# Optimization experiments

Hardware: AMD Instinct MI355X
Metric: run time of the kernel (lower is better)

Reference implementation:

```python
import jax, jax.numpy as jnp
import numpy as np

# Static module configuration (matches init_kwargs)
B, C_IN, H, W = 128, 64, 32, 32
C_OUT = 128
K = 3
PAD = 1
STRIDE = 1
OUT_H = (H + 2 * PAD - K) // STRIDE + 1  # 32
OUT_W = (W + 2 * PAD - K) // STRIDE + 1  # 32
L = OUT_H * OUT_W                        # 1024
IN_FEAT = C_IN * K * K                   # 576


def setup_inputs() -> dict:
    key = jax.random.key(0)
    k1, k2, k3 = jax.random.split(key, 3)
    x = jax.random.normal(k1, (B, C_IN, H, W), dtype=jnp.float32)
    # kaiming-uniform-ish scale: 1/sqrt(fan_in)
    bound = 1.0 / np.sqrt(IN_FEAT)
    weight = jax.random.uniform(k2, (L, IN_FEAT, C_OUT), dtype=jnp.float32,
                                minval=-bound, maxval=bound)
    bias = jax.random.uniform(k3, (L, C_OUT), dtype=jnp.float32,
                              minval=-bound, maxval=bound)
    return {"x": x, "weight": weight, "bias": bias}


def _unfold(x):
    """torch.nn.Unfold equivalent: returns (B, L, C*K*K), channel-major feature order."""
    xp = jnp.pad(x, ((0, 0), (0, 0), (PAD, PAD), (PAD, PAD)))
    cols = []
    for i in range(K):
        for j in range(K):
            cols.append(xp[:, :, i:i + OUT_H * STRIDE:STRIDE,
                               j:j + OUT_W * STRIDE:STRIDE])
    # (B, C, K*K, out_h, out_w) -> feature index = c*K*K + i*K + j (torch unfold order)
    p = jnp.stack(cols, axis=2)
    p = p.reshape(x.shape[0], C_IN * K * K, L)
    return p.transpose(0, 2, 1)  # (B, L, in_feat)


def reference(x, weight, bias):
    patches = _unfold(x)                                  # (B, L, in_feat)
    out = jnp.einsum('bli,lio->blo', patches, weight)     # per-location matmul
    out = out + bias[None]                                # (B, L, out_ch)
    out = out.transpose(0, 2, 1).reshape(x.shape[0], C_OUT, OUT_H, OUT_W)
    out = jax.nn.relu(out)
    # MaxPool2d(2, 2)
    Bn = out.shape[0]
    out = out.reshape(Bn, C_OUT, OUT_H // 2, 2, OUT_W // 2, 2).max(axis=(3, 5))
    return out
```

## Files before the change

### kernel.cpp

```cpp
#include <hip/hip_runtime.h>

#define BB   128
#define CI   64
#define HH   32
#define WW   32
#define CO   128
#define IF   576
#define OW   32
#define XH   34
#define XW   34
#define XP_CB    (CI*BB)
#define XP_ELEMS ((size_t)XH*XW*CI*BB)
#define BKC  64
#define NCH  36
#define LDK  72
#define COB  64

#define BAR() asm volatile("s_waitcnt lgkmcnt(0)\n\ts_barrier" ::: "memory")

using short8 = __attribute__((ext_vector_type(8))) short;
using f32x4  = __attribute__((ext_vector_type(4))) float;

__device__ __forceinline__ unsigned short f2bf(float f) {
  union { float f; unsigned int u; } v; v.f = f;
  unsigned int u = v.u;
  u = (u + 0x7FFFu + ((u >> 16) & 1u)) >> 16;
  return (unsigned short)u;
}

__device__ __forceinline__ unsigned int cvt_pk_bf16(float lo, float hi) {
  unsigned int r;
  asm("v_cvt_pk_bf16_f32 %0, %1, %2" : "=v"(r) : "v"(lo), "v"(hi));
  return r;
}

__global__ __launch_bounds__(256) void transpose_x(
    const float* __restrict__ x, unsigned short* __restrict__ xp) {
  const int c = blockIdx.x >> 5;
  const int h = blockIdx.x & 31;
  __shared__ __align__(16) unsigned short tile[32][136];
  const int t = threadIdx.x;
  const int w = t & 31, b0 = t >> 5;
#pragma unroll
  for (int p = 0; p < 16; ++p) {
    int b = b0 + p * 8;
    float v = x[(((size_t)b * CI + c) * HH + h) * WW + w];
    tile[w][b] = f2bf(v);
  }
  __syncthreads();
  const int w2 = t >> 3;
  const int bb = (t & 7) * 16;
  const unsigned short* src = &tile[w2][bb];
  unsigned short* dst = xp + ((size_t)(h + 1) * XW + (w2 + 1)) * XP_CB + c * BB + bb;
  *(uint4*)(dst)     = *(const uint4*)(src);
  *(uint4*)(dst + 8) = *(const uint4*)(src + 8);

  if (blockIdx.x < 132) {
    int s = blockIdx.x, hh, wh;
    if (s < 34)      { hh = 0;  wh = s; }
    else if (s < 68) { hh = 33; wh = s - 34; }
    else             { int k = s - 68; hh = 1 + (k >> 1); wh = (k & 1) * 33; }
    uint4 z; z.x = z.y = z.z = z.w = 0u;
    uint4* p = (uint4*)(xp + ((size_t)hh * XW + wh) * XP_CB) + t;
#pragma unroll
    for (int q = 0; q < 4; ++q) p[q * 256] = z;
  }
}

__global__ __launch_bounds__(512, 4) void local_gemm_pool(
    const float* __restrict__ Wt, const float* __restrict__ bias,
    const unsigned short* __restrict__ xp, float* __restrict__ out) {
  __shared__ __align__(16) unsigned short Asl[2][BB][LDK];
  __shared__ __align__(16) unsigned short Bsl[2][COB][LDK];

  const int tid  = threadIdx.x;
  const int lane = tid & 63;
  const int wave = tid >> 6;

  const int bidx = blockIdx.x;
  const int x8 = bidx & 7, j = bidx >> 3;
  const int coh = j & 1;
  const int pw  = (j >> 1) & 15;
  const int ph  = 2 * x8 + (j >> 5);
  const int co0 = coh * COB;

  const int sa = tid & 127;
  const int ka = tid >> 7;
  const int sb = tid & 63;
  const int kb = tid >> 6;

  const int r16 = lane & 15;
  const int q8  = (lane >> 4) * 8;
  const int m0  = (wave >> 2) * 64;
  const int n0  = (wave & 3) * 16;

  f32x4 acc[4] = {};
  f32x4 rmx[4] = {};

  float          breg0[8], breg1[8];
  unsigned short areg0[16], areg1[16];

  auto issue = [&](int it, float* br, unsigned short* ar) {
    const int loc = it / 9, kc = it % 9;
    const int di = kc / 3, dj = kc % 3;
    const int oh = 2 * ph + (loc >> 1), ow = 2 * pw + (loc & 1);
    const int l  = oh * OW + ow;
    const float* wp = Wt + ((size_t)l * IF + (size_t)(kb * 8) * 9 + kc) * CO
                         + co0 + sb;
#pragma unroll
    for (int i = 0; i < 8; ++i) br[i] = wp[(size_t)i * 9 * CO];
    const unsigned short* ap = xp + ((size_t)(oh + di) * XW + (ow + dj)) * XP_CB
                                  + (ka * 16) * BB + sa;
#pragma unroll
    for (int i = 0; i < 16; ++i) ar[i] = ap[i * BB];
  };

  auto writeLds = [&](int it, const float* br, const unsigned short* ar) {
    const int bufI = it & 1;
    uint4 vb;
    vb.x = cvt_pk_bf16(br[0], br[1]);
    vb.y = cvt_pk_bf16(br[2], br[3]);
    vb.z = cvt_pk_bf16(br[4], br[5]);
    vb.w = cvt_pk_bf16(br[6], br[7]);
    *(uint4*)&Bsl[bufI][sb][kb * 8] = vb;
#pragma unroll
    for (int p = 0; p < 2; ++p) {
      short8 va;
#pragma unroll
      for (int i = 0; i < 8; ++i) va[i] = (short)ar[p * 8 + i];
      *(short8*)&Asl[bufI][sa][ka * 16 + p * 8] = va;
    }
  };

  auto computeChunk = [&](int it) {
    const int bufI = it & 1;
#pragma unroll
    for (int h = 0; h < 2; ++h) {
      const int col = h * 32 + q8;
      short8 af[4], bf;
#pragma unroll
      for (int tm = 0; tm < 4; ++tm)
        af[tm] = *(const short8*)&Asl[bufI][m0 + tm * 16 + r16][col];
      bf = *(const short8*)&Bsl[bufI][n0 + r16][col];
#pragma unroll
      for (int tm = 0; tm < 4; ++tm)
        acc[tm] = __builtin_amdgcn_mfma_f32_16x16x32_bf16(af[tm], bf, acc[tm], 0, 0, 0);
    }
  };

  auto finishLoc = [&](int loc) {
    const int oh = 2 * ph + (loc >> 1), ow = 2 * pw + (loc & 1);
    const int l  = oh * OW + ow;
    const float bv = bias[l * CO + co0 + n0 + r16];
#pragma unroll
    for (int tm = 0; tm < 4; ++tm)
#pragma unroll
      for (int e = 0; e < 4; ++e) {
        float v = acc[tm][e] + bv;
        v = v > 0.f ? v : 0.f;
        rmx[tm][e] = fmaxf(rmx[tm][e], v);
        acc[tm][e] = 0.f;
      }
  };

  issue(0, breg0, areg0);
  issue(1, breg1, areg1);
  writeLds(0, breg0, areg0);
  issue(2, breg0, areg0);
  BAR();

  for (int it2 = 0; it2 < NCH; it2 += 2) {
    computeChunk(it2);
    writeLds(it2 + 1, breg1, areg1);
    if (it2 + 3 < NCH) issue(it2 + 3, breg1, areg1);
    if (it2 % 9 == 8) finishLoc(it2 / 9);
    BAR();
    const int ito = it2 + 1;
    computeChunk(ito);
    if (ito + 1 < NCH) writeLds(ito + 1, breg0, areg0);
    if (ito + 3 < NCH) issue(ito + 3, breg0, areg0);
    if (ito % 9 == 8) finishLoc(ito / 9);
    BAR();
  }

  float* op = out + (ph * 16 + pw);
  const int col = co0 + n0 + r16;
#pragma unroll
  for (int tm = 0; tm < 4; ++tm)
#pragma unroll
    for (int e = 0; e < 4; ++e) {
      const int row = m0 + tm * 16 + (lane >> 4) * 4 + e;
      op[((size_t)row * CO + col) * 256] = rmx[tm][e];
    }
}

extern "C" void kernel_launch(void* const* d_in, const int* in_sizes, int n_in,
                              void* d_out, int out_size, void* d_ws, size_t ws_size,
                              hipStream_t stream) {
  (void)in_sizes; (void)n_in; (void)out_size; (void)ws_size;
  const float* x  = (const float*)d_in[0];
  const float* w  = (const float*)d_in[1];
  const float* bs = (const float*)d_in[2];
  float* out = (float*)d_out;
  unsigned short* xp = (unsigned short*)d_ws;

  transpose_x<<<dim3(CI * HH), dim3(256), 0, stream>>>(x, xp);
  local_gemm_pool<<<dim3(512), dim3(512), 0, stream>>>(w, bs, xp, out);
}
```

Baseline: 454.0 us.

## Reorder pooled-window slots to share input tiles across the four output locations

The loop now walks the 36 (location, tap) slots in an order grouped by input pixel, so each of the 16 distinct input positions in the 4x4 receptive field is loaded into LDS once and reused by every location that needs it. Previously 36 A tiles were loaded. Four accumulator sets are kept live, one per pooled location, and bias, ReLU and max-pool are applied once at the end. The loop is fully unrolled with constexpr schedule tables. The cost is higher accumulator register pressure, which may hurt occupancy at launch bounds 512,4.

```diff
diff --git a/kernel.cpp b/kernel.cpp
--- a/kernel.cpp
+++ b/kernel.cpp
@@ -11,15 +11,24 @@
 #define XW   34
 #define XP_CB    (CI*BB)
 #define XP_ELEMS ((size_t)XH*XW*CI*BB)
-#define BKC  64
-#define NCH  36
 #define LDK  72
 #define COB  64
+#define NSLOT 36
+#define NGRP  16
 
 #define BAR() asm volatile("s_waitcnt lgkmcnt(0)\n\ts_barrier" ::: "memory")
 
 using short8 = __attribute__((ext_vector_type(8))) short;
 using f32x4  = __attribute__((ext_vector_type(4))) float;
+
+__device__ constexpr int SLOC[NSLOT] = {0,0,1,0,1,1,0,2,0,1,2,3,0,1,2,3,1,3,
+                                        0,2,0,1,2,3,0,1,2,3,1,3,2,2,3,2,3,3};
+__device__ constexpr int STAP[NSLOT] = {0,1,0,2,1,2,3,0,4,3,1,0,5,4,2,1,5,2,
+                                        6,3,7,6,4,3,8,7,5,4,8,5,6,7,6,8,7,8};
+__device__ constexpr int GRP[NSLOT]  = {0,1,1,2,2,3,4,4,5,5,5,5,6,6,6,6,7,7,
+                                        8,8,9,9,9,9,10,10,10,10,11,11,12,13,13,14,14,15};
+__device__ constexpr bool ISLAST[NSLOT] = {1,0,1,0,1,1,0,1,0,0,0,1,0,0,0,1,0,1,
+                                           0,1,0,0,0,1,0,0,0,1,0,1,1,0,1,0,1,1};
 
 __device__ __forceinline__ unsigned short f2bf(float f) {
   union { float f; unsigned int u; } v; v.f = f;
@@ -94,28 +103,22 @@
   const int m0  = (wave >> 2) * 64;
   const int n0  = (wave & 3) * 16;
 
-  f32x4 acc[4] = {};
-  f32x4 rmx[4] = {};
+  f32x4 acc[4][4] = {};
 
   float          breg0[8], breg1[8];
-  unsigned short areg0[16], areg1[16];
-
-  auto issue = [&](int it, float* br, unsigned short* ar) {
-    const int loc = it / 9, kc = it % 9;
-    const int di = kc / 3, dj = kc % 3;
+  unsigned short areg[16];
+
+  auto issueB = [&](int it, float* br) {
+    const int loc = SLOC[it], kc = STAP[it];
     const int oh = 2 * ph + (loc >> 1), ow = 2 * pw + (loc & 1);
     const int l  = oh * OW + ow;
     const float* wp = Wt + ((size_t)l * IF + (size_t)(kb * 8) * 9 + kc) * CO
                          + co0 + sb;
 #pragma unroll
     for (int i = 0; i < 8; ++i) br[i] = wp[(size_t)i * 9 * CO];
-    const unsigned short* ap = xp + ((size_t)(oh + di) * XW + (ow + dj)) * XP_CB
-                                  + (ka * 16) * BB + sa;
-#pragma unroll
-    for (int i = 0; i < 16; ++i) ar[i] = ap[i * BB];
-  };
-
-  auto writeLds = [&](int it, const float* br, const unsigned short* ar) {
+  };
+
+  auto writeLdsB = [&](int it, const float* br) {
     const int bufI = it & 1;
     uint4 vb;
     vb.x = cvt_pk_bf16(br[0], br[1]);
@@ -123,74 +126,81 @@
     vb.z = cvt_pk_bf16(br[4], br[5]);
     vb.w = cvt_pk_bf16(br[6], br[7]);
     *(uint4*)&Bsl[bufI][sb][kb * 8] = vb;
+  };
+
+  auto issueA = [&](int g) {
+    const int u = g >> 2, v = g & 3;
+    const unsigned short* ap = xp + ((size_t)(2 * ph + u) * XW + (2 * pw + v)) * XP_CB
+                                  + (ka * 16) * BB + sa;
+#pragma unroll
+    for (int i = 0; i < 16; ++i) areg[i] = ap[i * BB];
+  };
+
+  auto writeLdsA = [&](int g) {
+    const int bufI = g & 1;
 #pragma unroll
     for (int p = 0; p < 2; ++p) {
       short8 va;
 #pragma unroll
-      for (int i = 0; i < 8; ++i) va[i] = (short)ar[p * 8 + i];
+      for (int i = 0; i < 8; ++i) va[i] = (short)areg[p * 8 + i];
       *(short8*)&Asl[bufI][sa][ka * 16 + p * 8] = va;
     }
   };
 
-  auto computeChunk = [&](int it) {
-    const int bufI = it & 1;
+  auto computeSlot = [&](int it) {
+    const int Ab = GRP[it] & 1, Bb = it & 1, loc = SLOC[it];
 #pragma unroll
     for (int h = 0; h < 2; ++h) {
       const int col = h * 32 + q8;
       short8 af[4], bf;
 #pragma unroll
       for (int tm = 0; tm < 4; ++tm)
-        af[tm] = *(const short8*)&Asl[bufI][m0 + tm * 16 + r16][col];
-      bf = *(const short8*)&Bsl[bufI][n0 + r16][col];
+        af[tm] = *(const short8*)&Asl[Ab][m0 + tm * 16 + r16][col];
+      bf = *(const short8*)&Bsl[Bb][n0 + r16][col];
 #pragma unroll
       for (int tm = 0; tm < 4; ++tm)
-        acc[tm] = __builtin_amdgcn_mfma_f32_16x16x32_bf16(af[tm], bf, acc[tm], 0, 0, 0);
-    }
-  };
-
-  auto finishLoc = [&](int loc) {
-    const int oh = 2 * ph + (loc >> 1), ow = 2 * pw + (loc & 1);
-    const int l  = oh * OW + ow;
-    const float bv = bias[l * CO + co0 + n0 + r16];
-#pragma unroll
-    for (int tm = 0; tm < 4; ++tm)
-#pragma unroll
-      for (int e = 0; e < 4; ++e) {
-        float v = acc[tm][e] + bv;
-        v = v > 0.f ? v : 0.f;
-        rmx[tm][e] = fmaxf(rmx[tm][e], v);
-        acc[tm][e] = 0.f;
-      }
-  };
-
-  issue(0, breg0, areg0);
-  issue(1, breg1, areg1);
-  writeLds(0, breg0, areg0);
-  issue(2, breg0, areg0);
+        acc[loc][tm] = __builtin_amdgcn_mfma_f32_16x16x32_bf16(
+            af[tm], bf, acc[loc][tm], 0, 0, 0);
+    }
+  };
+
+  issueA(0);
+  issueB(0, breg0);
+  issueB(1, breg1);
+  writeLdsA(0);
+  issueA(1);
+  writeLdsB(0, breg0);
+  issueB(2, breg0);
   BAR();
 
-  for (int it2 = 0; it2 < NCH; it2 += 2) {
-    computeChunk(it2);
-    writeLds(it2 + 1, breg1, areg1);
-    if (it2 + 3 < NCH) issue(it2 + 3, breg1, areg1);
-    if (it2 % 9 == 8) finishLoc(it2 / 9);
-    BAR();
-    const int ito = it2 + 1;
-    computeChunk(ito);
-    if (ito + 1 < NCH) writeLds(ito + 1, breg0, areg0);
-    if (ito + 3 < NCH) issue(ito + 3, breg0, areg0);
-    if (ito % 9 == 8) finishLoc(ito / 9);
-    BAR();
+#pragma unroll
+  for (int it = 0; it < NSLOT; ++it) {
+    computeSlot(it);
+    if (it + 1 < NSLOT) writeLdsB(it + 1, ((it + 1) & 1) ? breg1 : breg0);
+    if (it + 3 < NSLOT) issueB(it + 3, ((it + 3) & 1) ? breg1 : breg0);
+    if (ISLAST[it]) {
+      if (GRP[it] + 1 < NGRP) writeLdsA(GRP[it] + 1);
+      if (GRP[it] + 2 < NGRP) issueA(GRP[it] + 2);
+    }
+    if (it + 1 < NSLOT) BAR();
   }
 
+  const int col = co0 + n0 + r16;
+  const int l00 = (2 * ph) * OW + 2 * pw;
+  const float bv0 = bias[(size_t)l00 * CO + col];
+  const float bv1 = bias[(size_t)(l00 + 1) * CO + col];
+  const float bv2 = bias[(size_t)(l00 + OW) * CO + col];
+  const float bv3 = bias[(size_t)(l00 + OW + 1) * CO + col];
   float* op = out + (ph * 16 + pw);
-  const int col = co0 + n0 + r16;
 #pragma unroll
   for (int tm = 0; tm < 4; ++tm)
 #pragma unroll
     for (int e = 0; e < 4; ++e) {
       const int row = m0 + tm * 16 + (lane >> 4) * 4 + e;
-      op[((size_t)row * CO + col) * 256] = rmx[tm][e];
+      float v = fmaxf(fmaxf(acc[0][tm][e] + bv0, acc[1][tm][e] + bv1),
+                      fmaxf(acc[2][tm][e] + bv2, acc[3][tm][e] + bv3));
+      v = fmaxf(v, 0.f);
+      op[((size_t)row * CO + col) * 256] = v;
     }
 }
 
```

Result: no change. 455.0 us (+0.2%).
